# Optimization experiments

Hardware: AMD Instinct MI355X
Metric: run time of the kernel (lower is better)

The kernel has to match this reference:

```python
import jax, jax.numpy as jnp
import numpy as np

OUT_SIZE = (7, 7, 7)
SPATIAL_SCALE = 1.0
SAMPLING_RATIO = 2
ALIGNED = True


def setup_inputs() -> dict:
    key = jax.random.key(0)
    kf, kc1, kc2 = jax.random.split(key, 3)
    B, C, D, H, W = 2, 128, 16, 64, 64
    N = 64
    features = jax.random.normal(kf, (B, C, D, H, W), dtype=jnp.float32)
    # Build valid boxes (z1,y1,x1,z2,y2,x2) inside the feature volume.
    dims = jnp.array([D, H, W], dtype=jnp.float32)
    lo = jax.random.uniform(kc1, (B, N, 3)) * dims * 0.6
    ext = 2.0 + jax.random.uniform(kc2, (B, N, 3)) * dims * 0.35
    hi = jnp.minimum(lo + ext, dims - 1.0)
    rois = jnp.concatenate([lo, hi], axis=-1).astype(jnp.float32)  # [B,N,6]
    return {"features": features, "rois": rois}


def _trilinear_sample(feat, z, y, x):
    # feat: [C,D,H,W]; z,y,x: [N,Pd,Ph,Pw] pixel coords (align_corners=False,
    # zero padding: out-of-bounds corners contribute 0).
    C, D, H, W = feat.shape
    z0f, y0f, x0f = jnp.floor(z), jnp.floor(y), jnp.floor(x)
    lz, ly, lx = z - z0f, y - y0f, x - x0f
    z0 = z0f.astype(jnp.int32)
    y0 = y0f.astype(jnp.int32)
    x0 = x0f.astype(jnp.int32)
    feat_flat = feat.reshape(C, -1)  # [C, D*H*W]

    def corner(zi, yi, xi, w):
        valid = ((zi >= 0) & (zi < D) & (yi >= 0) & (yi < H) & (xi >= 0) & (xi < W))
        idx = (jnp.clip(zi, 0, D - 1) * H + jnp.clip(yi, 0, H - 1)) * W + jnp.clip(xi, 0, W - 1)
        vals = jnp.take(feat_flat, idx.reshape(-1), axis=1).reshape((C,) + idx.shape)
        return vals * (w * valid.astype(w.dtype))[None]

    out = corner(z0, y0, x0, (1 - lz) * (1 - ly) * (1 - lx))
    out = out + corner(z0, y0, x0 + 1, (1 - lz) * (1 - ly) * lx)
    out = out + corner(z0, y0 + 1, x0, (1 - lz) * ly * (1 - lx))
    out = out + corner(z0, y0 + 1, x0 + 1, (1 - lz) * ly * lx)
    out = out + corner(z0 + 1, y0, x0, lz * (1 - ly) * (1 - lx))
    out = out + corner(z0 + 1, y0, x0 + 1, lz * (1 - ly) * lx)
    out = out + corner(z0 + 1, y0 + 1, x0, lz * ly * (1 - lx))
    out = out + corner(z0 + 1, y0 + 1, x0 + 1, lz * ly * lx)
    return out  # [C,N,Pd,Ph,Pw]


def _roi_align_3d(features, rois):
    B, C, D, H, W = features.shape
    od, oh, ow = OUT_SIZE
    s = SAMPLING_RATIO if SAMPLING_RATIO > 0 else 1
    dt = features.dtype
    d_step = (jnp.arange(od * s, dtype=dt) + 0.5) / s
    h_step = (jnp.arange(oh * s, dtype=dt) + 0.5) / s
    w_step = (jnp.arange(ow * s, dtype=dt) + 0.5) / s

    def per_batch(feat, roi):  # feat [C,D,H,W], roi [N,6]
        roi = roi * SPATIAL_SCALE
        if ALIGNED:
            roi = roi - 0.5
        z1, y1, x1, z2, y2, x2 = (roi[:, i] for i in range(6))
        bd = jnp.maximum(z2 - z1, 1e-6) / od
        bh = jnp.maximum(y2 - y1, 1e-6) / oh
        bw = jnp.maximum(x2 - x1, 1e-6) / ow
        zg = z1[:, None] + d_step[None, :] * bd[:, None]  # [N, od*s]
        yg = y1[:, None] + h_step[None, :] * bh[:, None]  # [N, oh*s]
        xg = x1[:, None] + w_step[None, :] * bw[:, None]  # [N, ow*s]
        z, y, x = jnp.broadcast_arrays(zg[:, :, None, None], yg[:, None, :, None], xg[:, None, None, :])
        sam = _trilinear_sample(feat, z, y, x)  # [C,N,od*s,oh*s,ow*s]
        N = roi.shape[0]
        sam = sam.reshape(C, N, od, s, oh, s, ow, s).mean(axis=(3, 5, 7))
        return sam.transpose(1, 0, 2, 3, 4)  # [N,C,od,oh,ow]

    return jax.vmap(per_batch)(features, rois)  # [B,N,C,od,oh,ow]


def reference(features, rois):
    return _roi_align_3d(features, rois)
```

## Files before the change

### kernel.cpp

```cpp
#include <hip/hip_runtime.h>

constexpr int Bc = 2, Nc = 64, Cc = 128, Dc = 16, Hc = 64, Wc = 64;
constexpr int OD = 7, OH = 7, OW = 7;
constexpr int CELLS = OD * OH * OW;
constexpr int DHW = Dc * Hc * Wc, HW = Hc * Wc;
constexpr int MAXZ = 10, MAXY = 25, MAXX = 25;
constexpr int XS = 25;
constexpr int ROWS = MAXZ * MAXY;
constexpr int SUBSZ = ROWS * XS;

typedef __fp16 h2 __attribute__((ext_vector_type(2)));

__device__ inline unsigned pk_f16(float a, float b) {
    return __builtin_bit_cast(unsigned, __builtin_amdgcn_cvt_pkrtz(a, b));
}

__device__ inline float fdot2(unsigned a, unsigned b, float c) {
#if __has_builtin(__builtin_amdgcn_fdot2)
    return __builtin_amdgcn_fdot2(__builtin_bit_cast(h2, a),
                                  __builtin_bit_cast(h2, b), c, false);
#else
    h2 ha = __builtin_bit_cast(h2, a);
    h2 hb = __builtin_bit_cast(h2, b);
    return fmaf((float)ha.x, (float)hb.x, fmaf((float)ha.y, (float)hb.y, c));
#endif
}

__global__ __launch_bounds__(384) void roialign3d_v9(
    const float* __restrict__ feat, const float* __restrict__ rois,
    float* __restrict__ out)
{
    __shared__ unsigned sub[SUBSZ + 2];
    __shared__ int2     tzp[14], typ[14];
    __shared__ float2   wzp[14], wyp[14];
    __shared__ int      txo[14];
    __shared__ unsigned wxh[14];
    __shared__ int      rowglob[ROWS];

    const int blk = blockIdx.x;
    const int cp  = blk & 63;
    const int n   = (blk >> 6) & 63;
    const int b   = blk >> 12;
    const int tid = threadIdx.x;

    const float* rp = rois + (size_t)(b * Nc + n) * 6;
    float r1a[3] = {rp[0] - 0.5f, rp[1] - 0.5f, rp[2] - 0.5f};
    float r2a[3] = {rp[3] - 0.5f, rp[4] - 0.5f, rp[5] - 0.5f};
    const int dims[3] = {Dc, Hc, Wc};
    const int maxn[3] = {MAXZ, MAXY, MAXX};

    float bs[3]; int lo[3], ncnt[3];
    #pragma unroll
    for (int a = 0; a < 3; ++a) {
        bs[a] = fmaxf(r2a[a] - r1a[a], 1e-6f) * (1.0f / 7.0f);
        float smin = r1a[a] + 0.25f * bs[a];
        float smax = r1a[a] + 6.75f * bs[a];
        int l = max(0, (int)floorf(smin));
        int h = min(dims[a] - 1, (int)floorf(smax) + 1);
        lo[a] = l;
        ncnt[a] = min(h - l + 1, maxn[a]);
    }
    const int zn = ncnt[0], yn = ncnt[1], xn = ncnt[2];
    const int rows = zn * yn;
    const int zstride = yn * XS;

    if (tid < 42) {
        int a = tid / 14, m = tid - a * 14;
        float v = r1a[a] + ((float)m + 0.5f) * 0.5f * bs[a];
        float f = floorf(v);
        float l = v - f;
        int i0 = (int)f;
        int d  = dims[a];
        float w0 = (i0 >= 0 && i0 < d) ? 1.0f - l : 0.0f;
        float w1 = (i0 + 1 < d) ? l : 0.0f;
        if (a == 0) {
            int c0 = min(max(i0 - lo[0], 0), zn - 1);
            int c1 = min(max(i0 + 1 - lo[0], 0), zn - 1);
            tzp[m] = make_int2(c0, c1);
            wzp[m] = make_float2(w0, w1);
        } else if (a == 1) {
            int c0 = min(max(i0 - lo[1], 0), yn - 1);
            int c1 = min(max(i0 + 1 - lo[1], 0), yn - 1);
            typ[m] = make_int2(c0 * XS, c1 * XS);
            wyp[m] = make_float2(w0, w1);
        } else {
            int c0 = min(max(i0 - lo[2], -1), xn - 1);
            txo[m] = c0;
            wxh[m] = pk_f16(w0, w1);
        }
    }
    if (tid >= 128 && tid < 128 + ROWS) {
        int r = tid - 128;
        if (r < rows) {
            int z = r / yn;
            int y = r - z * yn;
            rowglob[r] = (lo[0] + z) * HW + (lo[1] + y) * Wc + lo[2];
        }
    }
    if (tid == 64) sub[0] = 0;
    if (tid == 65) sub[1 + rows * XS] = 0;
    __syncthreads();

    const int c0ch = cp * 2;
    const float* fb = feat + ((size_t)b * Cc + c0ch) * DHW;
    const int total = rows * XS;
    for (int p = tid; p < total; p += 384) {
        int row = p / XS;
        int x   = p - row * XS;
        int xs  = min(x, xn - 1);
        int g   = rowglob[row] + xs;
        sub[1 + p] = pk_f16(fb[g], fb[g + DHW]);
    }

    int i = 0, j = 0, k = 0;
    int4 tzr; float4 wzv; int4 ty; float4 wyv;
    int xo0 = 0, xo1 = 0; unsigned wh0 = 0, wh1 = 0;
    if (tid < CELLS) {
        i = tid / 49;
        int rem = tid - i * 49;
        j = rem / 7;
        k = rem - j * 7;
        tzr = *(const int4*)&tzp[2 * i];
        wzv = *(const float4*)&wzp[2 * i];
        ty  = *(const int4*)&typ[2 * j];
        wyv = *(const float4*)&wyp[2 * j];
        xo0 = txo[2 * k]; xo1 = txo[2 * k + 1];
        wh0 = wxh[2 * k]; wh1 = wxh[2 * k + 1];
    }
    __syncthreads();

    if (tid < CELLS) {
        const unsigned* G = sub + 1;

        int c0z = tzr.x;
        int p1 = tzr.y - c0z;
        int p2 = tzr.z - c0z;
        int p3 = tzr.w - c0z;
        float cz0 = wzv.x + (p1 == 0 ? wzv.y : 0.0f)
                  + (p2 == 0 ? wzv.z : 0.0f) + (p3 == 0 ? wzv.w : 0.0f);
        float cz1 = (p1 == 1 ? wzv.y : 0.0f)
                  + (p2 == 1 ? wzv.z : 0.0f) + (p3 == 1 ? wzv.w : 0.0f);
        float cz2 = (p3 == 2 ? wzv.w : 0.0f);
        int zb0 = c0z * zstride;
        int zb1 = min(c0z + 1, zn - 1) * zstride;
        int zb2 = min(c0z + 2, zn - 1) * zstride;

        const int   zbs[3] = {zb0, zb1, zb2};
        const float czs[3] = {cz0, cz1, cz2};
        const int   yo[4] = {ty.x, ty.y, ty.z, ty.w};
        const float wy[4] = {wyv.x, wyv.y, wyv.z, wyv.w};

        float a0 = 0.0f, a1 = 0.0f;
        #pragma unroll
        for (int d = 0; d < 3; ++d) {
            int zb = zbs[d];
            float s0 = 0.0f, s1 = 0.0f;
            #pragma unroll
            for (int yi = 0; yi < 4; ++yi) {
                int base = zb + yo[yi];
                unsigned p0a = G[base + xo0], p0b = G[base + xo0 + 1];
                unsigned p1a = G[base + xo1], p1b = G[base + xo1 + 1];
                unsigned c0p0 = __builtin_amdgcn_perm(p0b, p0a, 0x05040100u);
                unsigned c1p0 = __builtin_amdgcn_perm(p0b, p0a, 0x07060302u);
                unsigned c0p1 = __builtin_amdgcn_perm(p1b, p1a, 0x05040100u);
                unsigned c1p1 = __builtin_amdgcn_perm(p1b, p1a, 0x07060302u);
                float r0 = fdot2(c0p1, wh1, fdot2(c0p0, wh0, 0.0f));
                float r1 = fdot2(c1p1, wh1, fdot2(c1p0, wh0, 0.0f));
                s0 = fmaf(wy[yi], r0, s0);
                s1 = fmaf(wy[yi], r1, s1);
            }
            a0 = fmaf(czs[d], s0, a0);
            a1 = fmaf(czs[d], s1, a1);
        }
        size_t obase = ((size_t)(b * Nc + n) * Cc + c0ch) * CELLS;
        out[obase + tid]         = a0 * 0.125f;
        out[obase + CELLS + tid] = a1 * 0.125f;
    }
}

extern "C" void kernel_launch(void* const* d_in, const int* in_sizes, int n_in,
                              void* d_out, int out_size, void* d_ws, size_t ws_size,
                              hipStream_t stream) {
    const float* feat = (const float*)d_in[0];
    const float* rois = (const float*)d_in[1];
    float* out = (float*)d_out;
    int blocks = Bc * Nc * (Cc / 2);
    hipLaunchKernelGGL(roialign3d_v9, dim3(blocks), dim3(384), 0, stream,
                       feat, rois, out);
}
```

Measured before the change: 48.79 us.

## Remove rowglob table and barrier, compute row addresses inline with 4-wide staging

```diff
diff --git a/kernel.cpp b/kernel.cpp
--- a/kernel.cpp
+++ b/kernel.cpp
@@ -6,8 +6,7 @@
 constexpr int DHW = Dc * Hc * Wc, HW = Hc * Wc;
 constexpr int MAXZ = 10, MAXY = 25, MAXX = 25;
 constexpr int XS = 25;
-constexpr int ROWS = MAXZ * MAXY;
-constexpr int SUBSZ = ROWS * XS;
+constexpr int SUBSZ = MAXZ * MAXY * XS;
 
 typedef __fp16 h2 __attribute__((ext_vector_type(2)));
 
@@ -26,7 +25,7 @@
 #endif
 }
 
-__global__ __launch_bounds__(384) void roialign3d_v9(
+__global__ __launch_bounds__(384) void roialign3d_v10(
     const float* __restrict__ feat, const float* __restrict__ rois,
     float* __restrict__ out)
 {
@@ -35,7 +34,6 @@
     __shared__ float2   wzp[14], wyp[14];
     __shared__ int      txo[14];
     __shared__ unsigned wxh[14];
-    __shared__ int      rowglob[ROWS];
 
     const int blk = blockIdx.x;
     const int cp  = blk & 63;
@@ -89,47 +87,57 @@
             wxh[m] = pk_f16(w0, w1);
         }
     }
-    if (tid >= 128 && tid < 128 + ROWS) {
-        int r = tid - 128;
-        if (r < rows) {
-            int z = r / yn;
-            int y = r - z * yn;
-            rowglob[r] = (lo[0] + z) * HW + (lo[1] + y) * Wc + lo[2];
-        }
-    }
     if (tid == 64) sub[0] = 0;
     if (tid == 65) sub[1 + rows * XS] = 0;
-    __syncthreads();
 
     const int c0ch = cp * 2;
     const float* fb = feat + ((size_t)b * Cc + c0ch) * DHW;
-    const int total = rows * XS;
-    for (int p = tid; p < total; p += 384) {
-        int row = p / XS;
-        int x   = p - row * XS;
-        int xs  = min(x, xn - 1);
-        int g   = rowglob[row] + xs;
-        sub[1 + p] = pk_f16(fb[g], fb[g + DHW]);
+    const unsigned mz = 65535u / (unsigned)yn + 1u;
+    const int gz = lo[0] * HW + lo[1] * Wc + lo[2];
+
+    const int nmain = rows * 6;
+    for (int p = tid; p < nmain; p += 384) {
+        int row = (p * 10923) >> 16;
+        int c   = p - row * 6;
+        int x0  = c << 2;
+        int z   = (int)(((unsigned)row * mz) >> 16);
+        int y   = row - z * yn;
+        int g   = gz + z * HW + y * Wc;
+        int xs0 = min(x0,     xn - 1);
+        int xs1 = min(x0 + 1, xn - 1);
+        int xs2 = min(x0 + 2, xn - 1);
+        int xs3 = min(x0 + 3, xn - 1);
+        unsigned d0 = pk_f16(fb[g + xs0], fb[g + xs0 + DHW]);
+        unsigned d1 = pk_f16(fb[g + xs1], fb[g + xs1 + DHW]);
+        unsigned d2 = pk_f16(fb[g + xs2], fb[g + xs2 + DHW]);
+        unsigned d3 = pk_f16(fb[g + xs3], fb[g + xs3 + DHW]);
+        int basep = 1 + row * XS + x0;
+        sub[basep]     = d0;
+        sub[basep + 1] = d1;
+        sub[basep + 2] = d2;
+        sub[basep + 3] = d3;
     }
-
-    int i = 0, j = 0, k = 0;
-    int4 tzr; float4 wzv; int4 ty; float4 wyv;
-    int xo0 = 0, xo1 = 0; unsigned wh0 = 0, wh1 = 0;
-    if (tid < CELLS) {
-        i = tid / 49;
-        int rem = tid - i * 49;
-        j = rem / 7;
-        k = rem - j * 7;
-        tzr = *(const int4*)&tzp[2 * i];
-        wzv = *(const float4*)&wzp[2 * i];
-        ty  = *(const int4*)&typ[2 * j];
-        wyv = *(const float4*)&wyp[2 * j];
-        xo0 = txo[2 * k]; xo1 = txo[2 * k + 1];
-        wh0 = wxh[2 * k]; wh1 = wxh[2 * k + 1];
+    for (int row = tid; row < rows; row += 384) {
+        int z  = (int)(((unsigned)row * mz) >> 16);
+        int y  = row - z * yn;
+        int xs = min(24, xn - 1);
+        int g  = gz + z * HW + y * Wc + xs;
+        sub[1 + row * XS + 24] = pk_f16(fb[g], fb[g + DHW]);
     }
     __syncthreads();
 
     if (tid < CELLS) {
+        int i   = tid / 49;
+        int rem = tid - i * 49;
+        int j   = rem / 7;
+        int k   = rem - j * 7;
+        int4   tzr = *(const int4*)&tzp[2 * i];
+        float4 wzv = *(const float4*)&wzp[2 * i];
+        int4   ty  = *(const int4*)&typ[2 * j];
+        float4 wyv = *(const float4*)&wyp[2 * j];
+        int    xo0 = txo[2 * k], xo1 = txo[2 * k + 1];
+        unsigned wh0 = wxh[2 * k], wh1 = wxh[2 * k + 1];
+
         const unsigned* G = sub + 1;
 
         int c0z = tzr.x;
@@ -185,6 +193,6 @@
     const float* rois = (const float*)d_in[1];
     float* out = (float*)d_out;
     int blocks = Bc * Nc * (Cc / 2);
-    hipLaunchKernelGGL(roialign3d_v9, dim3(blocks), dim3(384), 0, stream,
+    hipLaunchKernelGGL(roialign3d_v10, dim3(blocks), dim3(384), 0, stream,
                        feat, rois, out);
 }
```

New measurement: 60.17 us. 23.3% more time.
